# Performance work log

Hardware: AMD Instinct MI355X
Metric: run time of the kernel (lower is better)

Reference implementation:

```python
import jax, jax.numpy as jnp
import numpy as np


def _iir_forward(b_coeff, rho, psi, u_in, y_init, u_init):
    # Coefficient computation: stable 2nd-order resonator parameterization
    r = jax.nn.sigmoid(rho)
    theta = jnp.pi * jax.nn.sigmoid(psi)
    a1 = -2.0 * r * jnp.cos(theta)
    a2 = r * r

    B, T = u_in.shape
    nb = b_coeff.shape[0]  # number of FIR taps (n_b)

    # FIR (moving-average) part, fully vectorized over batch and time:
    # v[t] = sum_k b[k] * u[t-k]; past inputs come from u_init = [u[-1], u[-2], ...]
    u_ext = jnp.concatenate([u_init[:, ::-1], u_in], axis=1)  # [B, T + nb - 1], time-ordered
    v = jnp.zeros_like(u_in)
    for k in range(nb):  # small fixed loop over filter taps
        v = v + b_coeff[k] * jax.lax.dynamic_slice_in_dim(u_ext, nb - 1 - k, T, axis=1)

    # AR (recursive) part: y[t] = v[t] - a1*y[t-1] - a2*y[t-2]  (sequential scan over time)
    def step(carry, v_t):
        y1, y2 = carry  # y[t-1], y[t-2], each [B]
        y = v_t - a1 * y1 - a2 * y2
        return (y, y1), y

    init = (y_init[:, 0], y_init[:, 1])  # [y[-1], y[-2]] per lfiltic convention
    _, y = jax.lax.scan(step, init, v.T)  # y: [T, B]
    return y.T  # [B, T]


def setup_inputs() -> dict:
    key = jax.random.key(0)
    k1, k2, k3, k4 = jax.random.split(key, 4)
    B, T, NB = 1024, 16384, 3
    return {
        "b_coeff": 0.1 * jax.random.normal(k1, (NB,), dtype=jnp.float32),
        "rho": jnp.asarray(jax.random.normal(k2, (), dtype=jnp.float32) + 0.9),
        "psi": jnp.asarray(jax.random.normal(k3, (), dtype=jnp.float32) * 0.5),
        "u_in": jax.random.normal(k4, (B, T), dtype=jnp.float32),
        "y_init": jnp.zeros((B, 2), dtype=jnp.float32),
        "u_init": jnp.zeros((B, NB - 1), dtype=jnp.float32),
    }


def reference(b_coeff, rho, psi, u_in, y_init, u_init):
    return _iir_forward(b_coeff, rho, psi, u_in, y_init, u_init)
```

## Files before the change

kernel.cpp:

```cpp
#include <hip/hip_runtime.h>
#include <math.h>


#define TLEN     16384
#define HALF     8192
#define NT       256
#define CK       32
#define NCH      256
#define SCAN_OFF   8450
#define CARRY_OFF  (SCAN_OFF + 2*NCH)
#define LDS_FLOATS (CARRY_OFF + 2)

__device__ __forceinline__ void mat2_sq(float& m00, float& m01, float& m10, float& m11) {
    float t00 = m00*m00 + m01*m10;
    float t01 = m00*m01 + m01*m11;
    float t10 = m10*m00 + m11*m10;
    float t11 = m10*m01 + m11*m11;
    m00 = t00; m01 = t01; m10 = t10; m11 = t11;
}

__global__ __launch_bounds__(NT, 4)
void iir_kernel(const float* __restrict__ bc,
                const float* __restrict__ rho_p,
                const float* __restrict__ psi_p,
                const float* __restrict__ u_in,
                const float* __restrict__ y_init,
                const float* __restrict__ u_init,
                float* __restrict__ y_out)
{
    __shared__ float lds[LDS_FLOATS];
    const int row = blockIdx.x;
    const int tid = threadIdx.x;

    const float rho = rho_p[0];
    const float psi = psi_p[0];
    const float r   = 1.0f / (1.0f + expf(-rho));
    const float th  = 3.14159265358979323846f / (1.0f + expf(-psi));
    const float a1  = -2.0f * r * cosf(th);
    const float a2  = r * r;
    const float b0  = bc[0], b1 = bc[1], b2 = bc[2];

    const float* urow = u_in  + (size_t)row * TLEN;
    float*       orow = y_out + (size_t)row * TLEN;

    for (int h = 0; h < 2; ++h) {
        const float* uh = urow + h * HALF;

        #pragma unroll
        for (int k = 0; k < 8; ++k) {
            int g = tid + k * NT;
            float4 uv = ((const float4*)uh)[g];
            int base = 4*g + 3 + (g >> 3);
            lds[base + 0] = uv.x;
            lds[base + 1] = uv.y;
            lds[base + 2] = uv.z;
            lds[base + 3] = uv.w;
        }
        if (tid == 0) {
            lds[0] = (h == 0) ? u_init[2*row + 1] : urow[h*HALF - 2];
            lds[1] = (h == 0) ? u_init[2*row + 0] : urow[h*HALF - 1];
        }
        __syncthreads();

        const int ub = 33 * tid;
        float um2 = lds[ub];
        float um1 = lds[ub + 1];
        float v[CK];
        float y1 = 0.0f, y2 = 0.0f;
        #pragma unroll
        for (int j = 0; j < CK; ++j) {
            float uc = lds[ub + 3 + j];
            float vv = fmaf(b2, um2, fmaf(b1, um1, b0 * uc));
            v[j] = vv;
            float y = fmaf(-a1, y1, fmaf(-a2, y2, vv));
            y2 = y1; y1 = y;
            um2 = um1; um1 = uc;
        }
        lds[SCAN_OFF + 2*tid]     = y1;
        lds[SCAN_OFF + 2*tid + 1] = y2;
        __syncthreads();

        if (tid < 64) {
            const int l = tid;
            float m00 = -a1, m01 = -a2, m10 = 1.0f, m11 = 0.0f;
            #pragma unroll
            for (int s = 0; s < 5; ++s) mat2_sq(m00, m01, m10, m11);

            float da[4], db[4];
            #pragma unroll
            for (int m = 0; m < 4; ++m) {
                da[m] = lds[SCAN_OFF + 8*l + 2*m];
                db[m] = lds[SCAN_OFF + 8*l + 2*m + 1];
            }

            float seed0 = 0.0f, seed1 = 0.0f;
            if (l == 0) {
                if (h == 0) { seed0 = y_init[2*row]; seed1 = y_init[2*row + 1]; }
                else        { seed0 = lds[CARRY_OFF]; seed1 = lds[CARRY_OFF + 1]; }
            }
            float s0 = seed0, s1 = seed1;
            #pragma unroll
            for (int m = 0; m < 4; ++m) {
                float n0 = fmaf(m00, s0, fmaf(m01, s1, da[m]));
                float n1 = fmaf(m10, s0, fmaf(m11, s1, db[m]));
                s0 = n0; s1 = n1;
            }
            float w00 = m00, w01 = m01, w10 = m10, w11 = m11;
            mat2_sq(w00, w01, w10, w11);
            mat2_sq(w00, w01, w10, w11);
            #pragma unroll
            for (int p = 0; p < 6; ++p) {
                float o0 = __shfl_up(s0, 1 << p);
                float o1 = __shfl_up(s1, 1 << p);
                if (l >= (1 << p)) {
                    s0 = fmaf(w00, o0, fmaf(w01, o1, s0));
                    s1 = fmaf(w10, o0, fmaf(w11, o1, s1));
                }
                if (p < 5) mat2_sq(w00, w01, w10, w11);
            }
            float p0 = __shfl_up(s0, 1);
            float p1 = __shfl_up(s1, 1);
            if (l == 0) { p0 = seed0; p1 = seed1; }
            float c0 = p0, c1 = p1;
            #pragma unroll
            for (int m = 0; m < 4; ++m) {
                lds[SCAN_OFF + 2*(4*l + m)]     = c0;
                lds[SCAN_OFF + 2*(4*l + m) + 1] = c1;
                float n0 = fmaf(m00, c0, fmaf(m01, c1, da[m]));
                float n1 = fmaf(m10, c0, fmaf(m11, c1, db[m]));
                c0 = n0; c1 = n1;
            }
        }
        __syncthreads();

        float y1f = lds[SCAN_OFF + 2*tid];
        float y2f = lds[SCAN_OFF + 2*tid + 1];
        #pragma unroll
        for (int j = 0; j < CK; ++j) {
            float y = fmaf(-a1, y1f, fmaf(-a2, y2f, v[j]));
            lds[ub + 3 + j] = y;
            y2f = y1f; y1f = y;
        }
        if (tid == NT - 1) {
            lds[CARRY_OFF]     = y1f;
            lds[CARRY_OFF + 1] = y2f;
        }
        __syncthreads();

        float* oh = orow + h * HALF;
        #pragma unroll
        for (int k = 0; k < 8; ++k) {
            int g = tid + k * NT;
            int base = 4*g + 3 + (g >> 3);
            float4 ov;
            ov.x = lds[base + 0];
            ov.y = lds[base + 1];
            ov.z = lds[base + 2];
            ov.w = lds[base + 3];
            ((float4*)oh)[g] = ov;
        }
        __syncthreads();
    }
}

extern "C" void kernel_launch(void* const* d_in, const int* in_sizes, int n_in,
                              void* d_out, int out_size, void* d_ws, size_t ws_size,
                              hipStream_t stream) {
    const float* bc    = (const float*)d_in[0];
    const float* rho   = (const float*)d_in[1];
    const float* psi   = (const float*)d_in[2];
    const float* u_in  = (const float*)d_in[3];
    const float* y_in  = (const float*)d_in[4];
    const float* u_ini = (const float*)d_in[5];
    float* y = (float*)d_out;
    const int B = in_sizes[3] / TLEN;
    iir_kernel<<<B, NT, 0, stream>>>(bc, rho, psi, u_in, y_in, u_ini, y);
}
```

Baseline: 123.3 us.

## Load and store each thread's chunk directly from global, dropping LDS staging

Measured after the change: 133.5 us. +8.2%, slower.

```diff
diff --git a/kernel.cpp b/kernel.cpp
--- a/kernel.cpp
+++ b/kernel.cpp
@@ -2,14 +2,12 @@
 #include <math.h>
 
 
-#define TLEN     16384
-#define HALF     8192
-#define NT       256
-#define CK       32
-#define NCH      256
-#define SCAN_OFF   8450
-#define CARRY_OFF  (SCAN_OFF + 2*NCH)
-#define LDS_FLOATS (CARRY_OFF + 2)
+#define TLEN  16384
+#define HALF  8192
+#define NT    256
+#define CK    32
+#define NCH   256
+#define CARRY (2*NCH)
 
 __device__ __forceinline__ void mat2_sq(float& m00, float& m01, float& m10, float& m11) {
     float t00 = m00*m00 + m01*m10;
@@ -28,7 +26,7 @@
                 const float* __restrict__ u_init,
                 float* __restrict__ y_out)
 {
-    __shared__ float lds[LDS_FLOATS];
+    __shared__ float sc[2*NCH + 2];
     const int row = blockIdx.x;
     const int tid = threadIdx.x;
 
@@ -44,40 +42,35 @@
     float*       orow = y_out + (size_t)row * TLEN;
 
     for (int h = 0; h < 2; ++h) {
-        const float* uh = urow + h * HALF;
+        const float* uc0 = urow + h * HALF + CK * tid;
 
+        float um2, um1;
+        if (tid == 0 && h == 0) {
+            um2 = u_init[2*row + 1];
+            um1 = u_init[2*row + 0];
+        } else {
+            float2 ub = *(const float2*)(uc0 - 2);
+            um2 = ub.x; um1 = ub.y;
+        }
+
+        float uu[CK];
         #pragma unroll
-        for (int k = 0; k < 8; ++k) {
-            int g = tid + k * NT;
-            float4 uv = ((const float4*)uh)[g];
-            int base = 4*g + 3 + (g >> 3);
-            lds[base + 0] = uv.x;
-            lds[base + 1] = uv.y;
-            lds[base + 2] = uv.z;
-            lds[base + 3] = uv.w;
-        }
-        if (tid == 0) {
-            lds[0] = (h == 0) ? u_init[2*row + 1] : urow[h*HALF - 2];
-            lds[1] = (h == 0) ? u_init[2*row + 0] : urow[h*HALF - 1];
-        }
-        __syncthreads();
+        for (int k = 0; k < CK/4; ++k)
+            *(float4*)&uu[4*k] = ((const float4*)uc0)[k];
 
-        const int ub = 33 * tid;
-        float um2 = lds[ub];
-        float um1 = lds[ub + 1];
         float v[CK];
         float y1 = 0.0f, y2 = 0.0f;
         #pragma unroll
         for (int j = 0; j < CK; ++j) {
-            float uc = lds[ub + 3 + j];
+            float uc = uu[j];
             float vv = fmaf(b2, um2, fmaf(b1, um1, b0 * uc));
             v[j] = vv;
             float y = fmaf(-a1, y1, fmaf(-a2, y2, vv));
             y2 = y1; y1 = y;
             um2 = um1; um1 = uc;
         }
-        lds[SCAN_OFF + 2*tid]     = y1;
-        lds[SCAN_OFF + 2*tid + 1] = y2;
+        sc[2*tid]     = y1;
+        sc[2*tid + 1] = y2;
         __syncthreads();
 
         if (tid < 64) {
@@ -89,14 +82,14 @@
             float da[4], db[4];
             #pragma unroll
             for (int m = 0; m < 4; ++m) {
-                da[m] = lds[SCAN_OFF + 8*l + 2*m];
-                db[m] = lds[SCAN_OFF + 8*l + 2*m + 1];
+                da[m] = sc[8*l + 2*m];
+                db[m] = sc[8*l + 2*m + 1];
             }
 
             float seed0 = 0.0f, seed1 = 0.0f;
             if (l == 0) {
                 if (h == 0) { seed0 = y_init[2*row]; seed1 = y_init[2*row + 1]; }
-                else        { seed0 = lds[CARRY_OFF]; seed1 = lds[CARRY_OFF + 1]; }
+                else        { seed0 = sc[CARRY]; seed1 = sc[CARRY + 1]; }
             }
             float s0 = seed0, s1 = seed1;
             #pragma unroll
@@ -124,8 +117,8 @@
             float c0 = p0, c1 = p1;
             #pragma unroll
             for (int m = 0; m < 4; ++m) {
-                lds[SCAN_OFF + 2*(4*l + m)]     = c0;
-                lds[SCAN_OFF + 2*(4*l + m) + 1] = c1;
+                sc[2*(4*l + m)]     = c0;
+                sc[2*(4*l + m) + 1] = c1;
                 float n0 = fmaf(m00, c0, fmaf(m01, c1, da[m]));
                 float n1 = fmaf(m10, c0, fmaf(m11, c1, db[m]));
                 c0 = n0; c1 = n1;
@@ -133,33 +126,24 @@
         }
         __syncthreads();
 
-        float y1f = lds[SCAN_OFF + 2*tid];
-        float y2f = lds[SCAN_OFF + 2*tid + 1];
+        float y1f = sc[2*tid];
+        float y2f = sc[2*tid + 1];
+        float* oc0 = orow + h * HALF + CK * tid;
+        float yy[CK];
         #pragma unroll
         for (int j = 0; j < CK; ++j) {
             float y = fmaf(-a1, y1f, fmaf(-a2, y2f, v[j]));
-            lds[ub + 3 + j] = y;
+            yy[j] = y;
             y2f = y1f; y1f = y;
         }
+        #pragma unroll
+        for (int k = 0; k < CK/4; ++k)
+            ((float4*)oc0)[k] = *(const float4*)&yy[4*k];
+
         if (tid == NT - 1) {
-            lds[CARRY_OFF]     = y1f;
-            lds[CARRY_OFF + 1] = y2f;
+            sc[CARRY]     = y1f;
+            sc[CARRY + 1] = y2f;
         }
-        __syncthreads();
-
-        float* oh = orow + h * HALF;
-        #pragma unroll
-        for (int k = 0; k < 8; ++k) {
-            int g = tid + k * NT;
-            int base = 4*g + 3 + (g >> 3);
-            float4 ov;
-            ov.x = lds[base + 0];
-            ov.y = lds[base + 1];
-            ov.z = lds[base + 2];
-            ov.w = lds[base + 3];
-            ((float4*)oh)[g] = ov;
-        }
-        __syncthreads();
     }
 }
 
```
